# Optimization experiments

Measured on AMD Instinct MI355X. Metric: run time of the kernel, lower is better.

Reference implementation:

```python
import jax, jax.numpy as jnp
import numpy as np

# dims
B, FIN, FOUT = 4, 64, 32
FMID = min(FIN, FOUT)          # fmiddle
NCLS, NH = 4, 64               # num_classes, SPADE nhidden
S = 32                         # D = H = W
EPS = 1e-5


def conv3d(x, w, b=None, pad=1):
    # x: [N,C,D,H,W], w: [O,I,kd,kh,kw]
    out = jax.lax.conv_general_dilated(
        x, w, window_strides=(1, 1, 1), padding=[(pad, pad)] * 3,
        dimension_numbers=('NCDHW', 'OIDHW', 'NCDHW'))
    if b is not None:
        out = out + b[None, :, None, None, None]
    return out


def instance_norm(x):
    # per-sample, per-channel over spatial dims (InstanceNorm3d, affine=False)
    mu = x.mean(axis=(2, 3, 4), keepdims=True)
    var = x.var(axis=(2, 3, 4), keepdims=True)
    return (x - mu) * jax.lax.rsqrt(var + EPS)


def spade(x, y, Ws, Bs, Wg, Bg, Wb, Bb):
    # x: [B,C,D,H,W]; param stacks have leading num_classes dim; y routes per sample.
    normalized = instance_norm(x)
    ws, bs, wg, bg, wb, bb = Ws[y], Bs[y], Wg[y], Bg[y], Wb[y], Bb[y]

    def one(xi, wsi, bsi, wgi, bgi, wbi, bbi):
        xi = xi[None]  # [1,C,D,H,W]
        actv = jax.nn.relu(conv3d(xi, wsi, bsi))
        gamma = conv3d(actv, wgi, bgi)[0]
        beta = conv3d(actv, wbi, bbi)[0]
        return gamma, beta

    gamma, beta = jax.vmap(one)(x, ws, bs, wg, bg, wb, bb)
    return normalized * (1.0 + gamma) + beta


def _lrelu(t):
    return jax.nn.leaky_relu(t, 0.2)


def setup_inputs() -> dict:
    key = jax.random.key(0)
    ks = jax.random.split(key, 24)
    sc = 0.05
    inp = {
        'x': jax.random.normal(ks[0], (B, FIN, S, S, S), jnp.float32),
        'y': jax.random.randint(ks[1], (B,), 0, NCLS, jnp.int64
                                if jax.config.jax_enable_x64 else jnp.int32),
        # SPADE norm_0 stacks: label_nc = norm_nc = FIN
        's0_ws': jax.random.normal(ks[2], (NCLS, NH, FIN, 3, 3, 3), jnp.float32) * sc,
        's0_bs': jnp.zeros((NCLS, NH), jnp.float32),
        's0_wg': jax.random.normal(ks[3], (NCLS, FIN, NH, 3, 3, 3), jnp.float32) * sc,
        's0_bg': jnp.zeros((NCLS, FIN), jnp.float32),
        's0_wb': jax.random.normal(ks[4], (NCLS, FIN, NH, 3, 3, 3), jnp.float32) * sc,
        's0_bb': jnp.zeros((NCLS, FIN), jnp.float32),
        # SPADE norm_1 stacks: label_nc = norm_nc = FMID
        's1_ws': jax.random.normal(ks[5], (NCLS, NH, FMID, 3, 3, 3), jnp.float32) * sc,
        's1_bs': jnp.zeros((NCLS, NH), jnp.float32),
        's1_wg': jax.random.normal(ks[6], (NCLS, FMID, NH, 3, 3, 3), jnp.float32) * sc,
        's1_bg': jnp.zeros((NCLS, FMID), jnp.float32),
        's1_wb': jax.random.normal(ks[7], (NCLS, FMID, NH, 3, 3, 3), jnp.float32) * sc,
        's1_bb': jnp.zeros((NCLS, FMID), jnp.float32),
        # resnet convs
        'conv0_w': jax.random.normal(ks[8], (FMID, FIN, 3, 3, 3), jnp.float32) * sc,
        'conv0_b': jnp.zeros((FMID,), jnp.float32),
        'conv1_w': jax.random.normal(ks[9], (FOUT, FMID, 3, 3, 3), jnp.float32) * sc,
        'conv1_b': jnp.zeros((FOUT,), jnp.float32),
        'convs_w': jax.random.normal(ks[10], (FOUT, FIN, 1, 1, 1), jnp.float32) * sc,
    }
    return inp


def reference(x, y, s0_ws, s0_bs, s0_wg, s0_bg, s0_wb, s0_bb,
              s1_ws, s1_bs, s1_wg, s1_bg, s1_wb, s1_bb,
              conv0_w, conv0_b, conv1_w, conv1_b, convs_w):
    x_s = conv3d(x, convs_w, None, pad=0)  # learned shortcut (fin != fout, no bias)
    dx = conv3d(_lrelu(spade(x, y, s0_ws, s0_bs, s0_wg, s0_bg, s0_wb, s0_bb)),
                conv0_w, conv0_b)
    dx = conv3d(_lrelu(spade(dx, y, s1_ws, s1_bs, s1_wg, s1_bg, s1_wb, s1_bb)),
                conv1_w, conv1_b)
    return x_s + dx
```

## Files before the change

kernel.cpp:

```cpp
#include <hip/hip_runtime.h>


#define S3 32768
constexpr float EPS = 1e-5f;

typedef __attribute__((ext_vector_type(8))) short s16x8;
typedef __attribute__((ext_vector_type(4))) float f32x4;
typedef __attribute__((ext_vector_type(16))) float f32x16;
typedef __attribute__((ext_vector_type(4))) unsigned short u16x4;
typedef __attribute__((ext_vector_type(8))) unsigned short u16x8;

#define GLL(g, l)                                                        \
  __builtin_amdgcn_global_load_lds(                                      \
      (const __attribute__((address_space(1))) void*)(g),                \
      (__attribute__((address_space(3))) void*)(l), 16, 0, 0)

__device__ __forceinline__ float bf2f(unsigned short u) {
  union { unsigned int i; float f; } v; v.i = ((unsigned int)u) << 16; return v.f;
}
__device__ __forceinline__ unsigned short f2bf(float f) {
  union { float f; unsigned int i; } v; v.f = f;
  unsigned int r = (v.i + 0x7FFFu + ((v.i >> 16) & 1u)) >> 16;
  return (unsigned short)r;
}

__global__ __launch_bounds__(256) void stats_kernel(const float* __restrict__ x,
                                                    float* __restrict__ mu,
                                                    float* __restrict__ rstd) {
  const int bc = blockIdx.x;
  const float* p = x + (size_t)bc * S3;
  float s = 0.f, s2 = 0.f;
  for (int i = threadIdx.x; i < S3 / 4; i += 256) {
    float4 v = reinterpret_cast<const float4*>(p)[i];
    s  += v.x + v.y + v.z + v.w;
    s2 += v.x * v.x + v.y * v.y + v.z * v.z + v.w * v.w;
  }
  for (int off = 32; off; off >>= 1) {
    s  += __shfl_down(s, off, 64);
    s2 += __shfl_down(s2, off, 64);
  }
  __shared__ float ls[4], ls2[4];
  const int wid = threadIdx.x >> 6;
  if ((threadIdx.x & 63) == 0) { ls[wid] = s; ls2[wid] = s2; }
  __syncthreads();
  if (threadIdx.x == 0) {
    float S = 0.f, S2 = 0.f;
    for (int i = 0; i < 4; ++i) { S += ls[i]; S2 += ls2[i]; }
    const float m = S / (float)S3;
    const float var = S2 / (float)S3 - m * m;
    mu[bc] = m;
    rstd[bc] = rsqrtf(var + EPS);
  }
}

__global__ __launch_bounds__(256) void stats_t32_p1(const short* __restrict__ t,
                                                    float* __restrict__ part) {
  const int b = blockIdx.y;
  const int chunk = blockIdx.x;
  const int tid = threadIdx.x;
  const int pq = tid & 3;
  float s[8], s2[8];
#pragma unroll
  for (int j = 0; j < 8; ++j) { s[j] = 0.f; s2[j] = 0.f; }
  const int vbase = chunk * 512;
#pragma unroll
  for (int v = tid >> 2; v < 512; v += 64) {
    u16x8 u = *reinterpret_cast<const u16x8*>(
        &t[((size_t)b * S3 + vbase + v) * 32 + pq * 8]);
#pragma unroll
    for (int j = 0; j < 8; ++j) { float f = bf2f(u[j]); s[j] += f; s2[j] += f * f; }
  }
#pragma unroll
  for (int off = 4; off < 64; off <<= 1) {
#pragma unroll
    for (int j = 0; j < 8; ++j) {
      s[j]  += __shfl_xor(s[j], off, 64);
      s2[j] += __shfl_xor(s2[j], off, 64);
    }
  }
  __shared__ float red[4][4][16];
  const int wv = tid >> 6, lane = tid & 63;
  if (lane < 4) {
#pragma unroll
    for (int j = 0; j < 8; ++j) { red[wv][lane][j] = s[j]; red[wv][lane][8 + j] = s2[j]; }
  }
  __syncthreads();
  if (tid < 32) {
    const int p = tid >> 3, j = tid & 7;
    float S = 0.f, S2 = 0.f;
#pragma unroll
    for (int w = 0; w < 4; ++w) { S += red[w][p][j]; S2 += red[w][p][8 + j]; }
    const int c = p * 8 + j;
    part[((size_t)(b * 64 + chunk)) * 64 + c] = S;
    part[((size_t)(b * 64 + chunk)) * 64 + 32 + c] = S2;
  }
}

__global__ __launch_bounds__(128) void stats_t32_p2(const float* __restrict__ part,
                                                    float* __restrict__ mu,
                                                    float* __restrict__ rstd) {
  const int tid = threadIdx.x;
  const int b = tid >> 5, c = tid & 31;
  float S = 0.f, S2 = 0.f;
#pragma unroll 4
  for (int k = 0; k < 64; ++k) {
    S  += part[((size_t)(b * 64 + k)) * 64 + c];
    S2 += part[((size_t)(b * 64 + k)) * 64 + 32 + c];
  }
  const float m = S / (float)S3;
  const float var = S2 / (float)S3 - m * m;
  mu[b * 32 + c] = m;
  rstd[b * 32 + c] = rsqrtf(var + EPS);
}

__global__ __launch_bounds__(256) void transpose_x(const float* __restrict__ x,
                                                   short* __restrict__ xt) {
  const int b = blockIdx.y;
  const int v0 = blockIdx.x * 64;
  __shared__ unsigned short t[64][72];
  const int vox = threadIdx.x & 63;
  const int cg = threadIdx.x >> 6;
#pragma unroll
  for (int k = 0; k < 16; ++k) {
    const int ci = cg * 16 + k;
    t[vox][ci] = f2bf(x[((size_t)(b * 64 + ci)) * S3 + v0 + vox]);
  }
  __syncthreads();
  const int vv = threadIdx.x >> 2, part = threadIdx.x & 3;
  uint4 u0 = *reinterpret_cast<const uint4*>(&t[vv][part * 16]);
  uint4 u1 = *reinterpret_cast<const uint4*>(&t[vv][part * 16 + 8]);
  short* dst = &xt[((size_t)(b * S3 + v0 + vv)) * 64 + part * 16];
  *reinterpret_cast<uint4*>(dst) = u0;
  *reinterpret_cast<uint4*>(dst + 8) = u1;
}

__global__ __launch_bounds__(256) void repack_w(
    const float* __restrict__ wA, const float* __restrict__ wB,
    short* __restrict__ dst, const int* __restrict__ y,
    int CBLK, int CO2, int CI, long clsA, long clsB, int paired, int total) {
  const int b = blockIdx.y;
  const int idx = blockIdx.x * 256 + threadIdx.x;
  if (idx >= total) return;
  const int cls = y[b];
  const int KCH = CI / 16;
  const int ci = idx & 15;
  const int co = (idx >> 4) % CO2;
  const int rest = idx / (16 * CO2);
  const int k16 = rest % KCH;
  const int tap = rest / KCH;
  const int srcch = k16 * 16 + ci;
  float v;
  if (paired) {
    const int H = CBLK >> 1;
    const int blk = co / CBLK, w = co % CBLK;
    if (w < H)
      v = wA[(size_t)clsA * cls + ((size_t)(blk * H + w) * CI + srcch) * 27 + tap];
    else
      v = wB[(size_t)clsB * cls + ((size_t)(blk * H + w - H) * CI + srcch) * 27 + tap];
  } else {
    v = wA[(size_t)clsA * cls + ((size_t)co * CI + srcch) * 27 + tap];
  }
  dst[(((size_t)(b * 27 + tap) * KCH + k16) * CO2 + co) * 16 + ci] = (short)f2bf(v);
}

template <int CIN, int CBLK, int COTOT, int EPI, int NNORM>
__global__ __launch_bounds__(256, 2) void conv_mfma(
    const short* __restrict__ xt,
    const short* __restrict__ W,
    const float* __restrict__ bias,
    int bias_stride,
    const int* __restrict__ y,
    const short* __restrict__ xnb,
    const float* __restrict__ mu,
    const float* __restrict__ rstd,
    const float* __restrict__ bgs,
    const float* __restrict__ bbs,
    const short* __restrict__ zp,
    float* __restrict__ outf,
    short* __restrict__ outb) {
  constexpr int KCH = CIN / 16;
  constexpr int NCOG = CBLK / 32;
  constexpr int WG = 9 * NCOG * 64;
  constexpr int WGP = ((WG + 255) / 256) * 256;
  constexpr int WISS = WGP / 256;

  __shared__ short ldsX[2048 * 8];
  __shared__ short ldsW[WGP * 8];

  const int tid = threadIdx.x;
  const int lane = tid & 63, wid = tid >> 6;
  const int l31 = lane & 31, khf = lane >> 5;
  const int b = blockIdx.y;
  const int cls = y[b];
  const int co_base = blockIdx.z * CBLK;
  const int tile = (blockIdx.x & 7) * 8 + (blockIdx.x >> 3);
  const int d0 = (tile >> 4) * 8, h0 = ((tile >> 2) & 3) * 8, w0 = (tile & 3) * 8;

  const short* gsrc[8];
#pragma unroll
  for (int k = 0; k < 8; ++k) {
    const int i = tid + k * 256;
    const int pl = i >> 10, slot = i & 1023;
    const short* g = zp;
    if (slot < 1000) {
      const int sd = slot / 100, r0 = slot - sd * 100;
      const int sh = r0 / 10, sw0 = r0 - sh * 10;
      const int gd = d0 + sd - 1, gh = h0 + sh - 1, gw = w0 + sw0 - 1;
      if ((unsigned)gd < 32u && (unsigned)gh < 32u && (unsigned)gw < 32u)
        g = xt + ((size_t)b * S3 + gd * 1024 + gh * 32 + gw) * CIN + pl * 8;
    }
    gsrc[k] = g;
  }

  auto stage_x = [&](int kc) {
#pragma unroll
    for (int k = 0; k < 8; ++k) {
      const int i = tid + k * 256;
      GLL(gsrc[k] + kc * 16, &ldsX[i * 8]);
    }
  };
  auto stage_w = [&](int kc, int kd) {
#pragma unroll
    for (int k = 0; k < WISS; ++k) {
      const int i = tid + k * 256;
      const short* g = zp;
      if (i < WG) {
        const int t9 = i / (NCOG * 64);
        const int r = i - t9 * (NCOG * 64);
        const int c = r >> 6, q = r & 63;
        g = W + (((size_t)(b * 27 + kd * 9 + t9) * KCH + kc) * COTOT +
                 co_base + c * 32 + (q & 31)) * 16 + (q >> 5) * 8;
      }
      GLL(g, &ldsW[i * 8]);
    }
  };

  f32x16 acc[4][NCOG];
#pragma unroll
  for (int v = 0; v < 4; ++v)
#pragma unroll
    for (int c = 0; c < NCOG; ++c)
#pragma unroll
      for (int r = 0; r < 16; ++r) acc[v][c][r] = 0.f;

  const int hw10 = (l31 >> 3) * 10 + (l31 & 7);
  const int xpl = khf * 1024;

#pragma unroll 1
  for (int kc = 0; kc < KCH; ++kc) {
#pragma unroll 1
    for (int kd = 0; kd < 3; ++kd) {
      __syncthreads();
      stage_w(kc, kd);
      if (kd == 0) stage_x(kc);
      __syncthreads();

      __builtin_amdgcn_s_setprio(1);
#pragma unroll
      for (int kh = 0; kh < 3; ++kh) {
#pragma unroll
        for (int kw = 0; kw < 3; ++kw) {
          const int t9 = kh * 3 + kw;
          s16x8 af[NCOG];
#pragma unroll
          for (int c = 0; c < NCOG; ++c)
            af[c] = *reinterpret_cast<const s16x8*>(
                &ldsW[((t9 * NCOG + c) * 64 + lane) * 8]);
          s16x8 bf[4];
#pragma unroll
          for (int vg = 0; vg < 4; ++vg) {
            const int slot = (2 * wid + (vg >> 1) + kd) * 100 +
                             ((vg & 1) * 4 + kh) * 10 + kw + hw10;
            bf[vg] = *reinterpret_cast<const s16x8*>(&ldsX[(xpl + slot) * 8]);
          }
#pragma unroll
          for (int c = 0; c < NCOG; ++c)
#pragma unroll
            for (int vg = 0; vg < 4; ++vg)
              acc[vg][c] = __builtin_amdgcn_mfma_f32_32x32x16_bf16(
                  af[c], bf[vg], acc[vg][c], 0, 0, 0);
        }
      }
      __builtin_amdgcn_s_setprio(0);
    }
  }

  const int vdb = d0 + 2 * wid;
  const int vhb = h0 + (l31 >> 3);
  const int vwb = w0 + (l31 & 7);

  if constexpr (EPI == 0 || EPI == 1) {
#pragma unroll
    for (int c = 0; c < NCOG; ++c)
#pragma unroll
      for (int q = 0; q < 4; ++q) {
        const int c0 = co_base + c * 32 + q * 8 + khf * 4;
        const f32x4 b4 = *reinterpret_cast<const f32x4*>(&bias[cls * bias_stride + c0]);
#pragma unroll
        for (int vg = 0; vg < 4; ++vg) {
          const int gv = (vdb + (vg >> 1)) * 1024 + (vhb + (vg & 1) * 4) * 32 + vwb;
          u16x4 o;
#pragma unroll
          for (int rr = 0; rr < 4; ++rr) {
            float v = acc[vg][c][q * 4 + rr] + b4[rr];
            if constexpr (EPI == 0) v = fmaxf(v, 0.f);
            o[rr] = f2bf(v);
          }
          *reinterpret_cast<u16x4*>(&outb[((size_t)b * S3 + gv) * COTOT + c0]) = o;
        }
      }
  }

  if constexpr (EPI == 2) {
    const int nb = blockIdx.z * 32;
#pragma unroll
    for (int q = 0; q < 4; ++q) {
      const int c0 = nb + q * 8 + khf * 4;
      const f32x4 m4  = *reinterpret_cast<const f32x4*>(&mu[b * NNORM + c0]);
      const f32x4 r4  = *reinterpret_cast<const f32x4*>(&rstd[b * NNORM + c0]);
      const f32x4 g4  = *reinterpret_cast<const f32x4*>(&bgs[cls * NNORM + c0]);
      const f32x4 bb4 = *reinterpret_cast<const f32x4*>(&bbs[cls * NNORM + c0]);
#pragma unroll
      for (int vg = 0; vg < 4; ++vg) {
        const int gv = (vdb + (vg >> 1)) * 1024 + (vhb + (vg & 1) * 4) * 32 + vwb;
        const size_t vgl = (size_t)b * S3 + gv;
        u16x4 u = *reinterpret_cast<const u16x4*>(&xnb[vgl * NNORM + c0]);
        u16x4 o;
#pragma unroll
        for (int rr = 0; rr < 4; ++rr) {
          const float gamma = acc[vg][0][q * 4 + rr] + g4[rr];
          const float beta  = acc[vg][1][q * 4 + rr] + bb4[rr];
          const float nrm = (bf2f(u[rr]) - m4[rr]) * r4[rr];
          float h = nrm * (1.f + gamma) + beta;
          h = h > 0.f ? h : 0.2f * h;
          o[rr] = f2bf(h);
        }
        *reinterpret_cast<u16x4*>(&outb[vgl * NNORM + c0]) = o;
      }
    }
  }

  if constexpr (EPI == 4) {
#pragma unroll
    for (int q = 0; q < 4; ++q) {
      const int c0 = q * 8 + khf * 4;
      const f32x4 b4 = *reinterpret_cast<const f32x4*>(&bias[c0]);
#pragma unroll
      for (int vg = 0; vg < 4; ++vg) {
        const int gv = (vdb + (vg >> 1)) * 1024 + (vhb + (vg & 1) * 4) * 32 + vwb;
#pragma unroll
        for (int rr = 0; rr < 4; ++rr) {
          float* p = &outf[((size_t)(b * 32 + c0 + rr)) * S3 + gv];
          *p += acc[vg][0][q * 4 + rr] + b4[rr];
        }
      }
    }
  }
}

__global__ __launch_bounds__(256) void shortcut_kernel(const float* __restrict__ x,
                                                       const float* __restrict__ wsc,
                                                       float* __restrict__ out) {
  const int b = blockIdx.y;
  const int v = blockIdx.x * 256 + threadIdx.x;
  __shared__ float lw[64 * 32];
  for (int i = threadIdx.x; i < 2048; i += 256) {
    int ci = i >> 5, o = i & 31;
    lw[i] = wsc[o * 64 + ci];
  }
  __syncthreads();
  float acc[32];
#pragma unroll
  for (int o = 0; o < 32; ++o) acc[o] = 0.f;
  const float* xp = x + (size_t)b * 64 * S3 + v;
#pragma unroll 1
  for (int ci = 0; ci < 64; ++ci) {
    const float xv = xp[(size_t)ci * S3];
    const float4* wp = reinterpret_cast<const float4*>(&lw[ci << 5]);
#pragma unroll
    for (int o4 = 0; o4 < 8; ++o4) {
      float4 w4 = wp[o4];
      acc[o4 * 4 + 0] += xv * w4.x;
      acc[o4 * 4 + 1] += xv * w4.y;
      acc[o4 * 4 + 2] += xv * w4.z;
      acc[o4 * 4 + 3] += xv * w4.w;
    }
  }
  float* op = out + (size_t)b * 32 * S3 + v;
#pragma unroll
  for (int o = 0; o < 32; ++o) op[(size_t)o * S3] = acc[o];
}

extern "C" void kernel_launch(void* const* d_in, const int* in_sizes, int n_in,
                              void* d_out, int out_size, void* d_ws, size_t ws_size,
                              hipStream_t stream) {
  const float* x       = (const float*)d_in[0];
  const int*   y       = (const int*)d_in[1];
  const float* s0_ws   = (const float*)d_in[2];
  const float* s0_bs   = (const float*)d_in[3];
  const float* s0_wg   = (const float*)d_in[4];
  const float* s0_bg   = (const float*)d_in[5];
  const float* s0_wb   = (const float*)d_in[6];
  const float* s0_bb   = (const float*)d_in[7];
  const float* s1_ws   = (const float*)d_in[8];
  const float* s1_bs   = (const float*)d_in[9];
  const float* s1_wg   = (const float*)d_in[10];
  const float* s1_bg   = (const float*)d_in[11];
  const float* s1_wb   = (const float*)d_in[12];
  const float* s1_bb   = (const float*)d_in[13];
  const float* conv0_w = (const float*)d_in[14];
  const float* conv0_b = (const float*)d_in[15];
  const float* conv1_w = (const float*)d_in[16];
  const float* conv1_b = (const float*)d_in[17];
  const float* convs_w = (const float*)d_in[18];

  float* out = (float*)d_out;
  char* ws = (char*)d_ws;
  short* xt    = (short*)(ws);
  short* actvT = (short*)(ws + 16777216);
  short* hT    = (short*)(ws + 33554432);
  short* d0T   = (short*)(ws + 50331648);
  short* Wa0   = (short*)(ws + 58720256);
  short* Ws0   = (short*)(ws + 60817408);
  short* Wc0   = (short*)(ws + 62914560);
  short* Wa1   = (short*)(ws + 65011712);
  short* Ws1   = (short*)(ws + 67108864);
  short* Wc1   = (short*)(ws + 69206016);
  short* zp    = (short*)(ws + 70254592);
  float* stats = (float*)(ws + 71303168);
  float* mu0 = stats, *rstd0 = stats + 256, *mu1 = stats + 512, *rstd1 = stats + 640;
  float* spart = stats + 1024;

  hipMemsetAsync(zp, 0, 4096, stream);

  transpose_x<<<dim3(512, 4), 256, 0, stream>>>(x, xt);
  stats_kernel<<<dim3(256), 256, 0, stream>>>(x, mu0, rstd0);

  repack_w<<<dim3(432, 4), 256, 0, stream>>>(s0_ws, nullptr, Wa0, y, 64, 64, 64,
                                             64L * 64 * 27, 0, 0, 110592);
  repack_w<<<dim3(864, 4), 256, 0, stream>>>(s0_wg, s0_wb, Ws0, y, 64, 128, 64,
                                             64L * 64 * 27, 64L * 64 * 27, 1, 221184);
  repack_w<<<dim3(216, 4), 256, 0, stream>>>(conv0_w, nullptr, Wc0, y, 32, 32, 64,
                                             0, 0, 0, 55296);
  repack_w<<<dim3(216, 4), 256, 0, stream>>>(s1_ws, nullptr, Wa1, y, 64, 64, 32,
                                             64L * 32 * 27, 0, 0, 55296);
  repack_w<<<dim3(432, 4), 256, 0, stream>>>(s1_wg, s1_wb, Ws1, y, 64, 64, 64,
                                             32L * 64 * 27, 32L * 64 * 27, 1, 110592);
  repack_w<<<dim3(108, 4), 256, 0, stream>>>(conv1_w, nullptr, Wc1, y, 32, 32, 32,
                                             0, 0, 0, 27648);

  conv_mfma<64, 64, 64, 0, 0><<<dim3(64, 4, 1), 256, 0, stream>>>(
      xt, Wa0, s0_bs, 64, y, nullptr, nullptr, nullptr, nullptr, nullptr, zp,
      nullptr, actvT);
  conv_mfma<64, 64, 128, 2, 64><<<dim3(64, 4, 2), 256, 0, stream>>>(
      actvT, Ws0, nullptr, 0, y, xt, mu0, rstd0, s0_bg, s0_bb, zp,
      nullptr, hT);
  conv_mfma<64, 32, 32, 1, 0><<<dim3(64, 4, 1), 256, 0, stream>>>(
      hT, Wc0, conv0_b, 0, y, nullptr, nullptr, nullptr, nullptr, nullptr, zp,
      nullptr, d0T);
  stats_t32_p1<<<dim3(64, 4), 256, 0, stream>>>(d0T, spart);
  stats_t32_p2<<<dim3(1), 128, 0, stream>>>(spart, mu1, rstd1);
  conv_mfma<32, 64, 64, 0, 0><<<dim3(64, 4, 1), 256, 0, stream>>>(
      d0T, Wa1, s1_bs, 64, y, nullptr, nullptr, nullptr, nullptr, nullptr, zp,
      nullptr, actvT);
  conv_mfma<64, 64, 64, 2, 32><<<dim3(64, 4, 1), 256, 0, stream>>>(
      actvT, Ws1, nullptr, 0, y, d0T, mu1, rstd1, s1_bg, s1_bb, zp,
      nullptr, hT);
  shortcut_kernel<<<dim3(128, 4), 256, 0, stream>>>(x, convs_w, out);
  conv_mfma<32, 32, 32, 4, 0><<<dim3(64, 4, 1), 256, 0, stream>>>(
      hT, Wc1, conv1_b, 0, y, nullptr, nullptr, nullptr, nullptr, nullptr, zp,
      out, nullptr);
}
```

Before: 284.8 us.

## Split-K two SPADE convolutions to double grid parallelism, combine partials separately

Two convolutions that previously launched only 256 blocks (64 tiles × 4 batches) are now split over the input-channel dimension into two halves. Each half writes its own bf16 partial sum, and a new elementwise kernel adds the partials and applies bias and ReLU, or the SPADE normalization with leaky ReLU. The aim is to fill more compute units on the GPU. In exchange it adds extra global memory traffic and kernel launches, and rounds the partial sums to bf16 before they are added.

Result: slower. 303.5 us (+6.6%).

```diff
diff --git a/kernel.cpp b/kernel.cpp
--- a/kernel.cpp
+++ b/kernel.cpp
@@ -163,7 +163,59 @@
   dst[(((size_t)(b * 27 + tap) * KCH + k16) * CO2 + co) * 16 + ci] = (short)f2bf(v);
 }
 
-template <int CIN, int CBLK, int COTOT, int EPI, int NNORM>
+__global__ __launch_bounds__(256) void combine_actv(
+    const short* __restrict__ P0, const short* __restrict__ P1,
+    const float* __restrict__ bias, const int* __restrict__ y,
+    short* __restrict__ dst) {
+  const int b = blockIdx.y;
+  const int cls = y[b];
+  const size_t e = ((size_t)blockIdx.x * 256 + threadIdx.x) * 8;
+  const int c = (int)(e & 63);
+  const size_t g = (size_t)b * S3 * 64 + e;
+  u16x8 a = *reinterpret_cast<const u16x8*>(&P0[g]);
+  u16x8 bb = *reinterpret_cast<const u16x8*>(&P1[g]);
+  u16x8 o;
+#pragma unroll
+  for (int j = 0; j < 8; ++j) {
+    float v = bf2f(a[j]) + bf2f(bb[j]) + bias[cls * 64 + c + j];
+    o[j] = f2bf(fmaxf(v, 0.f));
+  }
+  *reinterpret_cast<u16x8*>(&dst[g]) = o;
+}
+
+__global__ __launch_bounds__(256) void combine_spade(
+    const short* __restrict__ P0, const short* __restrict__ P1,
+    const short* __restrict__ xn, const float* __restrict__ mu,
+    const float* __restrict__ rstd, const float* __restrict__ bgs,
+    const float* __restrict__ bbs, const int* __restrict__ y,
+    short* __restrict__ dst) {
+  const int b = blockIdx.y;
+  const int cls = y[b];
+  const int idx = blockIdx.x * 256 + threadIdx.x;
+  const int v = idx >> 2, part = idx & 2, c = (idx & 3) * 8;
+  (void)part;
+  const size_t b64 = ((size_t)b * S3 + v) * 64;
+  const size_t b32 = ((size_t)b * S3 + v) * 32;
+  u16x8 g0 = *reinterpret_cast<const u16x8*>(&P0[b64 + c]);
+  u16x8 g1 = *reinterpret_cast<const u16x8*>(&P1[b64 + c]);
+  u16x8 t0 = *reinterpret_cast<const u16x8*>(&P0[b64 + 32 + c]);
+  u16x8 t1 = *reinterpret_cast<const u16x8*>(&P1[b64 + 32 + c]);
+  u16x8 x8 = *reinterpret_cast<const u16x8*>(&xn[b32 + c]);
+  u16x8 o;
+#pragma unroll
+  for (int j = 0; j < 8; ++j) {
+    const int ch = c + j;
+    const float gamma = bf2f(g0[j]) + bf2f(g1[j]) + bgs[cls * 32 + ch];
+    const float beta  = bf2f(t0[j]) + bf2f(t1[j]) + bbs[cls * 32 + ch];
+    const float nrm = (bf2f(x8[j]) - mu[b * 32 + ch]) * rstd[b * 32 + ch];
+    float h = nrm * (1.f + gamma) + beta;
+    h = h > 0.f ? h : 0.2f * h;
+    o[j] = f2bf(h);
+  }
+  *reinterpret_cast<u16x8*>(&dst[b32 + c]) = o;
+}
+
+template <int CIN, int CBLK, int COTOT, int EPI, int NNORM, int KSPL = 1>
 __global__ __launch_bounds__(256, 2) void conv_mfma(
     const short* __restrict__ xt,
     const short* __restrict__ W,
@@ -177,7 +229,8 @@
     const float* __restrict__ bbs,
     const short* __restrict__ zp,
     float* __restrict__ outf,
-    short* __restrict__ outb) {
+    short* __restrict__ outb,
+    short* __restrict__ outb2) {
   constexpr int KCH = CIN / 16;
   constexpr int NCOG = CBLK / 32;
   constexpr int WG = 9 * NCOG * 64;
@@ -192,7 +245,8 @@
   const int l31 = lane & 31, khf = lane >> 5;
   const int b = blockIdx.y;
   const int cls = y[b];
-  const int co_base = blockIdx.z * CBLK;
+  const int co_base = (KSPL == 1) ? blockIdx.z * CBLK : 0;
+  const int kc0 = (KSPL == 1) ? 0 : blockIdx.z * (KCH / KSPL);
   const int tile = (blockIdx.x & 7) * 8 + (blockIdx.x >> 3);
   const int d0 = (tile >> 4) * 8, h0 = ((tile >> 2) & 3) * 8, w0 = (tile & 3) * 8;
 
@@ -247,7 +301,8 @@
   const int xpl = khf * 1024;
 
 #pragma unroll 1
-  for (int kc = 0; kc < KCH; ++kc) {
+  for (int kci = 0; kci < KCH / KSPL; ++kci) {
+    const int kc = kc0 + kci;
 #pragma unroll 1
     for (int kd = 0; kd < 3; ++kd) {
       __syncthreads();
@@ -343,7 +398,7 @@
   if constexpr (EPI == 4) {
 #pragma unroll
     for (int q = 0; q < 4; ++q) {
-      const int c0 = q * 8 + khf * 4;
+      const int c0 = co_base + q * 8 + khf * 4;
       const f32x4 b4 = *reinterpret_cast<const f32x4*>(&bias[c0]);
 #pragma unroll
       for (int vg = 0; vg < 4; ++vg) {
@@ -355,6 +410,24 @@
         }
       }
     }
+  }
+
+  if constexpr (EPI == 5) {
+    short* dst = blockIdx.z ? outb2 : outb;
+#pragma unroll
+    for (int c = 0; c < NCOG; ++c)
+#pragma unroll
+      for (int q = 0; q < 4; ++q) {
+        const int c0 = c * 32 + q * 8 + khf * 4;
+#pragma unroll
+        for (int vg = 0; vg < 4; ++vg) {
+          const int gv = (vdb + (vg >> 1)) * 1024 + (vhb + (vg & 1) * 4) * 32 + vwb;
+          u16x4 o;
+#pragma unroll
+          for (int rr = 0; rr < 4; ++rr) o[rr] = f2bf(acc[vg][c][q * 4 + rr]);
+          *reinterpret_cast<u16x4*>(&dst[((size_t)b * S3 + gv) * COTOT + c0]) = o;
+        }
+      }
   }
 }
 
@@ -430,6 +503,7 @@
   float* stats = (float*)(ws + 71303168);
   float* mu0 = stats, *rstd0 = stats + 256, *mu1 = stats + 512, *rstd1 = stats + 640;
   float* spart = stats + 1024;
+  short* Pext  = (short*)(ws + 71434240);
 
   hipMemsetAsync(zp, 0, 4096, stream);
 
@@ -449,25 +523,28 @@
   repack_w<<<dim3(108, 4), 256, 0, stream>>>(conv1_w, nullptr, Wc1, y, 32, 32, 32,
                                              0, 0, 0, 27648);
 
-  conv_mfma<64, 64, 64, 0, 0><<<dim3(64, 4, 1), 256, 0, stream>>>(
-      xt, Wa0, s0_bs, 64, y, nullptr, nullptr, nullptr, nullptr, nullptr, zp,
-      nullptr, actvT);
+  conv_mfma<64, 64, 64, 5, 0, 2><<<dim3(64, 4, 2), 256, 0, stream>>>(
+      xt, Wa0, nullptr, 0, y, nullptr, nullptr, nullptr, nullptr, nullptr, zp,
+      nullptr, hT, Pext);
+  combine_actv<<<dim3(1024, 4), 256, 0, stream>>>(hT, Pext, s0_bs, y, actvT);
   conv_mfma<64, 64, 128, 2, 64><<<dim3(64, 4, 2), 256, 0, stream>>>(
       actvT, Ws0, nullptr, 0, y, xt, mu0, rstd0, s0_bg, s0_bb, zp,
-      nullptr, hT);
+      nullptr, hT, nullptr);
   conv_mfma<64, 32, 32, 1, 0><<<dim3(64, 4, 1), 256, 0, stream>>>(
       hT, Wc0, conv0_b, 0, y, nullptr, nullptr, nullptr, nullptr, nullptr, zp,
-      nullptr, d0T);
+      nullptr, d0T, nullptr);
   stats_t32_p1<<<dim3(64, 4), 256, 0, stream>>>(d0T, spart);
   stats_t32_p2<<<dim3(1), 128, 0, stream>>>(spart, mu1, rstd1);
   conv_mfma<32, 64, 64, 0, 0><<<dim3(64, 4, 1), 256, 0, stream>>>(
       d0T, Wa1, s1_bs, 64, y, nullptr, nullptr, nullptr, nullptr, nullptr, zp,
-      nullptr, actvT);
-  conv_mfma<64, 64, 64, 2, 32><<<dim3(64, 4, 1), 256, 0, stream>>>(
-      actvT, Ws1, nullptr, 0, y, d0T, mu1, rstd1, s1_bg, s1_bb, zp,
-      nullptr, hT);
+      nullptr, actvT, nullptr);
+  conv_mfma<64, 64, 64, 5, 0, 2><<<dim3(64, 4, 2), 256, 0, stream>>>(
+      actvT, Ws1, nullptr, 0, y, nullptr, nullptr, nullptr, nullptr, nullptr, zp,
+      nullptr, xt, Pext);
+  combine_spade<<<dim3(512, 4), 256, 0, stream>>>(xt, Pext, d0T, mu1, rstd1,
+                                                  s1_bg, s1_bb, y, hT);
   shortcut_kernel<<<dim3(128, 4), 256, 0, stream>>>(x, convs_w, out);
   conv_mfma<32, 32, 32, 4, 0><<<dim3(64, 4, 1), 256, 0, stream>>>(
       hT, Wc1, conv1_b, 0, y, nullptr, nullptr, nullptr, nullptr, nullptr, zp,
-      out, nullptr);
-}
+      out, nullptr, nullptr);
+}
```
